# Kernel tuning notes

Hardware: AMD Instinct MI355X
Metric: run time of the kernel (lower is better)

## Reference

```python
import jax, jax.numpy as jnp
import numpy as np

EMBED_DIM = 1024
NUM_HEADS = 16
HEAD_DIM = EMBED_DIM // NUM_HEADS
SCALE = HEAD_DIM ** -0.5
B, S = 2, 2048


def setup_inputs() -> dict:
    key = jax.random.key(0)
    ks = jax.random.split(key, 10)
    def lin(kw, kb, fan_in):
        bound = 1.0 / np.sqrt(fan_in)
        W = jax.random.uniform(kw, (EMBED_DIM, EMBED_DIM), jnp.float32, -bound, bound)
        b = jax.random.uniform(kb, (EMBED_DIM,), jnp.float32, -bound, bound)
        return W, b
    Wq, bq = lin(ks[0], ks[1], EMBED_DIM)
    Wk, bk = lin(ks[2], ks[3], EMBED_DIM)
    Wv, bv = lin(ks[4], ks[5], EMBED_DIM)
    Wo, bo = lin(ks[6], ks[7], EMBED_DIM)
    x = jax.random.normal(ks[8], (B, S, EMBED_DIM), jnp.float32)
    # sparsity_mask: True where token kept (rand > sparsity with sparsity=0.5)
    sparsity_mask = jax.random.randint(ks[9], (B, NUM_HEADS, S), 0, 2).astype(bool)
    return {"x": x, "sparsity_mask": sparsity_mask,
            "Wq": Wq, "bq": bq, "Wk": Wk, "bk": bk,
            "Wv": Wv, "bv": bv, "Wo": Wo, "bo": bo}


def reference(x, sparsity_mask, Wq, bq, Wk, bk, Wv, bv, Wo, bo):
    b, s, _ = x.shape
    def heads(W, bias):
        # torch Linear: x @ W.T + b ; then [b, s, h, d] -> [b, h, s, d]
        y = x @ W.T + bias
        return y.reshape(b, s, NUM_HEADS, HEAD_DIM).transpose(0, 2, 1, 3)
    q = heads(Wq, bq)
    k = heads(Wk, bk)
    v = heads(Wv, bv)
    m = sparsity_mask[..., None].astype(q.dtype)  # [b, h, s, 1]
    q = q * m
    k = k * m
    attn = jnp.einsum('bhqd,bhkd->bhqk', q, k) * SCALE
    attn = jax.nn.softmax(attn, axis=-1)
    out = jnp.einsum('bhqk,bhkd->bhqd', attn, v)
    out = out.transpose(0, 2, 1, 3).reshape(b, s, EMBED_DIM)
    return out @ Wo.T + bo
```

## Files before the change

### kernel.cpp

```cpp
#include <hip/hip_runtime.h>

#define DEV __device__ __forceinline__

typedef __bf16 bf16x8 __attribute__((ext_vector_type(8)));
typedef __bf16 bf16x4 __attribute__((ext_vector_type(4)));
typedef float f32x4 __attribute__((ext_vector_type(4)));
typedef unsigned u32x4 __attribute__((ext_vector_type(4)));
typedef unsigned short ushort_t;

static constexpr int EMBED = 1024;
static constexpr int NHEAD = 16;
static constexpr int HDIM  = 64;
static constexpr int S_    = 2048;
static constexpr float SCALE_L2E = 0.125f * 1.44269504088896340736f;

DEV ushort_t f2bf(float f) {
  unsigned u = __builtin_bit_cast(unsigned, f);
  unsigned r = (u + 0x7fffu + ((u >> 16) & 1u)) >> 16;
  return (ushort_t)r;
}

#define GLOAD_LDS16(g, l)                                                   \
  __builtin_amdgcn_global_load_lds(                                         \
      (const __attribute__((address_space(1))) unsigned int*)(g),           \
      (__attribute__((address_space(3))) unsigned int*)(l), 16, 0, 0)

#define DRAIN_VM() asm volatile("s_waitcnt vmcnt(0)" ::: "memory")

__global__ __launch_bounds__(256) void convert_kernel(
    const float* __restrict__ x,
    const float* __restrict__ wq, const float* __restrict__ wk,
    const float* __restrict__ wv, const float* __restrict__ wo,
    ushort_t* __restrict__ xb, ushort_t* __restrict__ wqb,
    ushort_t* __restrict__ wkb, ushort_t* __restrict__ wvb,
    ushort_t* __restrict__ wob) {
  size_t i = ((size_t)blockIdx.x * blockDim.x + threadIdx.x) * 4;
  const float* src; ushort_t* dst; size_t off;
  if (i < 4194304u)      { src = x;  dst = xb;  off = i; }
  else if (i < 5242880u) { src = wq; dst = wqb; off = i - 4194304u; }
  else if (i < 6291456u) { src = wk; dst = wkb; off = i - 5242880u; }
  else if (i < 7340032u) { src = wv; dst = wvb; off = i - 6291456u; }
  else                   { src = wo; dst = wob; off = i - 7340032u; }
  float4 v = *(const float4*)(src + off);
  ushort4 o;
  o.x = f2bf(v.x); o.y = f2bf(v.y); o.z = f2bf(v.z); o.w = f2bf(v.w);
  *(ushort4*)(dst + off) = o;
}

__global__ __launch_bounds__(256) void qkv_kernel(
    const ushort_t* __restrict__ xb, const ushort_t* __restrict__ wqb,
    const ushort_t* __restrict__ wkb, const ushort_t* __restrict__ wvb,
    const float* __restrict__ bq, const float* __restrict__ bk,
    const float* __restrict__ bv, const int* __restrict__ mask,
    ushort_t* __restrict__ qo, ushort_t* __restrict__ ko,
    ushort_t* __restrict__ vto) {
  __shared__ __align__(16) unsigned char ldsA[16384];
  __shared__ __align__(16) unsigned char ldsB[16384];
  __shared__ float maskf[2][128];

  const int bid  = blockIdx.x;
  const int tid  = threadIdx.x;
  const int lane = tid & 63;
  const int w    = tid >> 6;
  const int wm   = (w >> 1) * 64;
  const int wn   = (w & 1) * 64;
  const int rl   = lane & 15;
  const int kg   = lane >> 4;

  int mode, ar0, br0;
  const ushort_t *A, *Bm;
  const float* bias;
  if (bid < 512) {
    mode = bid >> 8;
    int t = bid & 255;
    ar0 = (t & 31) * 128;
    br0 = (t >> 5) * 128;
    A = xb; Bm = mode ? wkb : wqb; bias = mode ? bk : bq;
  } else {
    mode = 2;
    int t = bid - 512;
    ar0 = (t & 7) * 128;
    br0 = (t >> 3) * 128;
    A = wvb; Bm = xb; bias = bv;
  }

  if (mode < 2) {
    int hl = tid >> 7, sl = tid & 127;
    int m = ar0 + sl;
    int b = m >> 11, s = m & 2047;
    int h = (br0 >> 6) + hl;
    maskf[hl][sl] = (float)mask[((size_t)b * NHEAD + h) * S_ + s];
  }

  f32x4 acc[4][4];
#pragma unroll
  for (int i = 0; i < 4; ++i)
#pragma unroll
    for (int j = 0; j < 4; ++j) acc[i][j] = f32x4{0.f, 0.f, 0.f, 0.f};

  auto STAGE = [&](int kt) {
    const int k0 = kt * 64;
#pragma unroll
    for (int s = 0; s < 8; ++s) {
      const int basev = s * 256 + w * 64;
      const int Lb = basev & 1023;
      const int L = Lb + lane;
      const int row = L >> 3;
      const int gu = (L & 7) ^ (row & 7);
      if (s < 4) {
        GLOAD_LDS16(A + (size_t)(ar0 + row) * EMBED + k0 + gu * 8, &ldsA[Lb * 16]);
      } else {
        GLOAD_LDS16(Bm + (size_t)(br0 + row) * EMBED + k0 + gu * 8, &ldsB[Lb * 16]);
      }
    }
  };

  for (int kt = 0; kt < 16; ++kt) {
    if (kt) __syncthreads();
    STAGE(kt);
    DRAIN_VM();
    __syncthreads();
#pragma unroll
    for (int kk = 0; kk < 2; ++kk) {
      bf16x8 af[4], bfr[4];
#pragma unroll
      for (int mb = 0; mb < 4; ++mb) {
        const int row = wm + mb * 16 + rl;
        const int off = (kk * 64 + kg * 16) ^ ((row & 7) << 4);
        af[mb] = *(const bf16x8*)(ldsA + row * 128 + off);
      }
#pragma unroll
      for (int nb = 0; nb < 4; ++nb) {
        const int row = wn + nb * 16 + rl;
        const int off = (kk * 64 + kg * 16) ^ ((row & 7) << 4);
        bfr[nb] = *(const bf16x8*)(ldsB + row * 128 + off);
      }
#pragma unroll
      for (int mb = 0; mb < 4; ++mb)
#pragma unroll
        for (int nb = 0; nb < 4; ++nb)
          acc[mb][nb] = __builtin_amdgcn_mfma_f32_16x16x32_bf16(
              af[mb], bfr[nb], acc[mb][nb], 0, 0, 0);
    }
  }

#pragma unroll
  for (int mb = 0; mb < 4; ++mb)
#pragma unroll
    for (int nb = 0; nb < 4; ++nb)
#pragma unroll
      for (int r = 0; r < 4; ++r) {
        int row_l = wm + mb * 16 + kg * 4 + r;
        int col_l = wn + nb * 16 + rl;
        float v = acc[mb][nb][r];
        if (mode < 2) {
          int m = ar0 + row_l, n = br0 + col_l;
          v = (v + bias[n]) * maskf[col_l >> 6][row_l];
          if (mode == 0) v *= SCALE_L2E;
          int b = m >> 11, s = m & 2047, h = n >> 6, d = n & 63;
          ushort_t* o = mode ? ko : qo;
          o[(((size_t)(b * NHEAD + h)) * S_ + s) * HDIM + d] = f2bf(v);
        } else {
          int n = ar0 + row_l, m = br0 + col_l;
          v += bias[n];
          int b = m >> 11, s = m & 2047, h = n >> 6, d = n & 63;
          vto[(((size_t)(b * NHEAD + h)) * HDIM + d) * S_ + s] = f2bf(v);
        }
      }
}

__global__ __launch_bounds__(256) void gemm_o_kernel(
    const ushort_t* __restrict__ A, const ushort_t* __restrict__ Bm,
    const float* __restrict__ bias, float* __restrict__ outp) {
  __shared__ __align__(16) unsigned char ldsA[16384];
  __shared__ __align__(16) unsigned char ldsB[16384];

  const int tid  = threadIdx.x;
  const int lane = tid & 63;
  const int w    = tid >> 6;
  const int ar0  = blockIdx.x * 128;
  const int br0  = blockIdx.y * 128;
  const int wm   = (w >> 1) * 64;
  const int wn   = (w & 1) * 64;
  const int rl   = lane & 15;
  const int kg   = lane >> 4;

  f32x4 acc[4][4];
#pragma unroll
  for (int i = 0; i < 4; ++i)
#pragma unroll
    for (int j = 0; j < 4; ++j) acc[i][j] = f32x4{0.f, 0.f, 0.f, 0.f};

  auto STAGE = [&](int kt) {
    const int k0 = kt * 64;
#pragma unroll
    for (int s = 0; s < 8; ++s) {
      const int basev = s * 256 + w * 64;
      const int Lb = basev & 1023;
      const int L = Lb + lane;
      const int row = L >> 3;
      const int gu = (L & 7) ^ (row & 7);
      if (s < 4) {
        GLOAD_LDS16(A + (size_t)(ar0 + row) * EMBED + k0 + gu * 8, &ldsA[Lb * 16]);
      } else {
        GLOAD_LDS16(Bm + (size_t)(br0 + row) * EMBED + k0 + gu * 8, &ldsB[Lb * 16]);
      }
    }
  };

  for (int kt = 0; kt < 16; ++kt) {
    if (kt) __syncthreads();
    STAGE(kt);
    DRAIN_VM();
    __syncthreads();
#pragma unroll
    for (int kk = 0; kk < 2; ++kk) {
      bf16x8 af[4], bfr[4];
#pragma unroll
      for (int mb = 0; mb < 4; ++mb) {
        const int row = wm + mb * 16 + rl;
        const int off = (kk * 64 + kg * 16) ^ ((row & 7) << 4);
        af[mb] = *(const bf16x8*)(ldsA + row * 128 + off);
      }
#pragma unroll
      for (int nb = 0; nb < 4; ++nb) {
        const int row = wn + nb * 16 + rl;
        const int off = (kk * 64 + kg * 16) ^ ((row & 7) << 4);
        bfr[nb] = *(const bf16x8*)(ldsB + row * 128 + off);
      }
#pragma unroll
      for (int mb = 0; mb < 4; ++mb)
#pragma unroll
        for (int nb = 0; nb < 4; ++nb)
          acc[mb][nb] = __builtin_amdgcn_mfma_f32_16x16x32_bf16(
              af[mb], bfr[nb], acc[mb][nb], 0, 0, 0);
    }
  }

#pragma unroll
  for (int mb = 0; mb < 4; ++mb)
#pragma unroll
    for (int nb = 0; nb < 4; ++nb)
#pragma unroll
      for (int r = 0; r < 4; ++r) {
        int m = ar0 + wm + mb * 16 + kg * 4 + r;
        int n = br0 + wn + nb * 16 + rl;
        outp[(size_t)m * EMBED + n] = acc[mb][nb][r] + bias[n];
      }
}

__global__ __launch_bounds__(512) void attn_kernel(
    const ushort_t* __restrict__ qp, const ushort_t* __restrict__ kp,
    const ushort_t* __restrict__ vtp, ushort_t* __restrict__ ao) {
  __shared__ __align__(16) unsigned char ldsK[3][8192];
  __shared__ __align__(16) unsigned char ldsV[3][8192];
  __shared__ __align__(16) unsigned char ldsP[8][2048];

  const int bid  = blockIdx.x;
  const int bh   = (bid & 7) * 4 + (bid >> 7);
  const int qt   = (bid >> 3) & 15;
  const int tid  = threadIdx.x;
  const int lane = tid & 63;
  const int w    = tid >> 6;
  const int q0   = qt * 128 + w * 16;
  const int rl   = lane & 15;
  const int kg   = lane >> 4;
  const int pswz = (rl & 7) << 4;

  const bf16x8 ones = __builtin_bit_cast(bf16x8,
      u32x4{0x3F803F80u, 0x3F803F80u, 0x3F803F80u, 0x3F803F80u});

  bf16x8 qa[2];
#pragma unroll
  for (int kk = 0; kk < 2; ++kk)
    qa[kk] = *(const bf16x8*)(qp + ((size_t)bh * S_ + q0 + rl) * HDIM +
                              kk * 32 + kg * 8);

  f32x4 o_acc[4];
  f32x4 o_l = f32x4{0.f, 0.f, 0.f, 0.f};
#pragma unroll
  for (int nb = 0; nb < 4; ++nb) o_acc[nb] = f32x4{0.f, 0.f, 0.f, 0.f};

  unsigned char* pb = ldsP[w];

  auto STAGE = [&](int kt, int slot) {
#pragma unroll
    for (int s = 0; s < 2; ++s) {
      const int Lb = w * 64;
      const int L = Lb + lane;
      const int row = L >> 3;
      const int gu = (L & 7) ^ (row & 7);
      if (s == 0) {
        GLOAD_LDS16(kp + ((size_t)bh * S_ + (size_t)kt * 64 + row) * HDIM + gu * 8,
                    &ldsK[slot][L * 16]);
      } else {
        GLOAD_LDS16(vtp + ((size_t)bh * HDIM + row) * S_ + (size_t)kt * 64 + gu * 8,
                    &ldsV[slot][L * 16]);
      }
    }
  };

  STAGE(0, 0);
  STAGE(1, 1);
  asm volatile("s_waitcnt vmcnt(2) lgkmcnt(0)" ::: "memory");
  __builtin_amdgcn_s_barrier();
  int cur = 0;
  for (int kt = 0; kt < 32; ++kt) {
    if (kt + 2 < 32) {
      int slot = cur + 2; if (slot >= 3) slot -= 3;
      STAGE(kt + 2, slot);
    }

    f32x4 sa[4];
#pragma unroll
    for (int nb = 0; nb < 4; ++nb) sa[nb] = f32x4{0.f, 0.f, 0.f, 0.f};
    __builtin_amdgcn_s_setprio(1);
#pragma unroll
    for (int nb = 0; nb < 4; ++nb) {
      const int row = nb * 16 + rl;
#pragma unroll
      for (int kk = 0; kk < 2; ++kk) {
        bf16x8 kf = *(const bf16x8*)(ldsK[cur] + row * 128 +
                                     ((kk * 64 + kg * 16) ^ ((row & 7) << 4)));
        sa[nb] = __builtin_amdgcn_mfma_f32_16x16x32_bf16(kf, qa[kk], sa[nb], 0, 0, 0);
      }
    }
    __builtin_amdgcn_s_setprio(0);

#pragma unroll
    for (int nb = 0; nb < 4; ++nb) {
      bf16x4 pk4;
#pragma unroll
      for (int r = 0; r < 4; ++r)
        pk4[r] = (__bf16)__builtin_amdgcn_exp2f(sa[nb][r]);
      *(bf16x4*)(pb + rl * 128 + ((nb * 32 + kg * 8) ^ pswz)) = pk4;
    }
    asm volatile("s_waitcnt lgkmcnt(0)" ::: "memory");
    __builtin_amdgcn_sched_barrier(0);

    bf16x8 pa[2];
#pragma unroll
    for (int kk = 0; kk < 2; ++kk)
      pa[kk] = *(const bf16x8*)(pb + rl * 128 + ((kk * 64 + kg * 16) ^ pswz));

    __builtin_amdgcn_s_setprio(1);
    o_l = __builtin_amdgcn_mfma_f32_16x16x32_bf16(pa[0], ones, o_l, 0, 0, 0);
    o_l = __builtin_amdgcn_mfma_f32_16x16x32_bf16(pa[1], ones, o_l, 0, 0, 0);

#pragma unroll
    for (int nb = 0; nb < 4; ++nb) {
      const int row = nb * 16 + rl;
#pragma unroll
      for (int kk = 0; kk < 2; ++kk) {
        bf16x8 vb = *(const bf16x8*)(ldsV[cur] + row * 128 +
                                     ((kk * 64 + kg * 16) ^ ((row & 7) << 4)));
        o_acc[nb] = __builtin_amdgcn_mfma_f32_16x16x32_bf16(pa[kk], vb, o_acc[nb], 0, 0, 0);
      }
    }
    __builtin_amdgcn_s_setprio(0);

    if (kt + 2 < 32) {
      asm volatile("s_waitcnt vmcnt(2) lgkmcnt(0)" ::: "memory");
    } else {
      asm volatile("s_waitcnt vmcnt(0) lgkmcnt(0)" ::: "memory");
    }
    __builtin_amdgcn_s_barrier();
    cur = (cur == 2) ? 0 : cur + 1;
  }

  const int b = bh >> 4, h = bh & 15;
#pragma unroll
  for (int r = 0; r < 4; ++r) {
    float linv = 1.0f / o_l[r];
    const int row = q0 + kg * 4 + r;
#pragma unroll
    for (int nb = 0; nb < 4; ++nb) {
      float v = o_acc[nb][r] * linv;
      ao[((size_t)b * S_ + row) * EMBED + h * HDIM + nb * 16 + rl] = f2bf(v);
    }
  }
}

extern "C" void kernel_launch(void* const* d_in, const int* in_sizes, int n_in,
                              void* d_out, int out_size, void* d_ws, size_t ws_size,
                              hipStream_t stream) {
  const float* x    = (const float*)d_in[0];
  const int*   mask = (const int*)d_in[1];
  const float* Wq   = (const float*)d_in[2];
  const float* bq   = (const float*)d_in[3];
  const float* Wk   = (const float*)d_in[4];
  const float* bk   = (const float*)d_in[5];
  const float* Wv   = (const float*)d_in[6];
  const float* bv   = (const float*)d_in[7];
  const float* Wo   = (const float*)d_in[8];
  const float* bo   = (const float*)d_in[9];

  char* ws = (char*)d_ws;
  ushort_t* xb  = (ushort_t*)(ws);
  ushort_t* wqb = (ushort_t*)(ws + 8388608);
  ushort_t* wkb = (ushort_t*)(ws + 10485760);
  ushort_t* wvb = (ushort_t*)(ws + 12582912);
  ushort_t* wob = (ushort_t*)(ws + 14680064);
  ushort_t* qb  = (ushort_t*)(ws + 16777216);
  ushort_t* kb  = (ushort_t*)(ws + 25165824);
  ushort_t* vtb = (ushort_t*)(ws + 33554432);
  ushort_t* aob = (ushort_t*)(ws + 41943040);

  hipLaunchKernelGGL(convert_kernel, dim3(8192), dim3(256), 0, stream,
                     x, Wq, Wk, Wv, Wo, xb, wqb, wkb, wvb, wob);
  hipLaunchKernelGGL(qkv_kernel, dim3(768), dim3(256), 0, stream,
                     xb, wqb, wkb, wvb, bq, bk, bv, mask, qb, kb, vtb);
  hipLaunchKernelGGL(attn_kernel, dim3(512), dim3(512), 0, stream,
                     qb, kb, vtb, aob);
  hipLaunchKernelGGL(gemm_o_kernel, dim3(32, 8), dim3(256), 0, stream,
                     aob, wob, bo, (float*)d_out);
}
```

Measured before the change: 115.2 us.

## Process two KV tiles per iteration with four-slot LDS ring buffer

The attention main loop now handles two 64-key tiles per iteration. Both QK^T products are issued up front, then the exp/write of the first tile's P is interleaved with the second tile's softmax and the PV products. The K/V LDS ring grows from three to four slots, and loads for the next pair are issued after a barrier at the end of each pair. The aim is to halve the per-tile barrier and wait overhead and give the MFMA unit more independent work to overlap with exp and LDS traffic. In exchange it raises register pressure and LDS use, and it moves the prefetch issue to the end of the compute phase.

```diff
diff --git a/kernel.cpp b/kernel.cpp
--- a/kernel.cpp
+++ b/kernel.cpp
@@ -252,8 +252,8 @@
 __global__ __launch_bounds__(512) void attn_kernel(
     const ushort_t* __restrict__ qp, const ushort_t* __restrict__ kp,
     const ushort_t* __restrict__ vtp, ushort_t* __restrict__ ao) {
-  __shared__ __align__(16) unsigned char ldsK[3][8192];
-  __shared__ __align__(16) unsigned char ldsV[3][8192];
+  __shared__ __align__(16) unsigned char ldsK[4][8192];
+  __shared__ __align__(16) unsigned char ldsV[4][8192];
   __shared__ __align__(16) unsigned char ldsP[8][2048];
 
   const int bid  = blockIdx.x;
@@ -300,33 +300,19 @@
     }
   };
 
-  STAGE(0, 0);
-  STAGE(1, 1);
-  asm volatile("s_waitcnt vmcnt(2) lgkmcnt(0)" ::: "memory");
-  __builtin_amdgcn_s_barrier();
-  int cur = 0;
-  for (int kt = 0; kt < 32; ++kt) {
-    if (kt + 2 < 32) {
-      int slot = cur + 2; if (slot >= 3) slot -= 3;
-      STAGE(kt + 2, slot);
-    }
-
-    f32x4 sa[4];
-#pragma unroll
-    for (int nb = 0; nb < 4; ++nb) sa[nb] = f32x4{0.f, 0.f, 0.f, 0.f};
-    __builtin_amdgcn_s_setprio(1);
+  auto QK = [&](int slot, f32x4 sa[4]) {
 #pragma unroll
     for (int nb = 0; nb < 4; ++nb) {
       const int row = nb * 16 + rl;
 #pragma unroll
       for (int kk = 0; kk < 2; ++kk) {
-        bf16x8 kf = *(const bf16x8*)(ldsK[cur] + row * 128 +
+        bf16x8 kf = *(const bf16x8*)(ldsK[slot] + row * 128 +
                                      ((kk * 64 + kg * 16) ^ ((row & 7) << 4)));
         sa[nb] = __builtin_amdgcn_mfma_f32_16x16x32_bf16(kf, qa[kk], sa[nb], 0, 0, 0);
       }
     }
-    __builtin_amdgcn_s_setprio(0);
-
+  };
+  auto SMW = [&](const f32x4 sa[4]) {
 #pragma unroll
     for (int nb = 0; nb < 4; ++nb) {
       bf16x4 pk4;
@@ -335,37 +321,65 @@
         pk4[r] = (__bf16)__builtin_amdgcn_exp2f(sa[nb][r]);
       *(bf16x4*)(pb + rl * 128 + ((nb * 32 + kg * 8) ^ pswz)) = pk4;
     }
+  };
+  auto PVL = [&](int slot) {
+    bf16x8 pa[2];
+#pragma unroll
+    for (int kk = 0; kk < 2; ++kk)
+      pa[kk] = *(const bf16x8*)(pb + rl * 128 + ((kk * 64 + kg * 16) ^ pswz));
+    o_l = __builtin_amdgcn_mfma_f32_16x16x32_bf16(pa[0], ones, o_l, 0, 0, 0);
+    o_l = __builtin_amdgcn_mfma_f32_16x16x32_bf16(pa[1], ones, o_l, 0, 0, 0);
+#pragma unroll
+    for (int nb = 0; nb < 4; ++nb) {
+      const int row = nb * 16 + rl;
+#pragma unroll
+      for (int kk = 0; kk < 2; ++kk) {
+        bf16x8 vb = *(const bf16x8*)(ldsV[slot] + row * 128 +
+                                     ((kk * 64 + kg * 16) ^ ((row & 7) << 4)));
+        o_acc[nb] = __builtin_amdgcn_mfma_f32_16x16x32_bf16(pa[kk], vb, o_acc[nb], 0, 0, 0);
+      }
+    }
+  };
+
+  STAGE(0, 0); STAGE(1, 1); STAGE(2, 2); STAGE(3, 3);
+  asm volatile("s_waitcnt vmcnt(4) lgkmcnt(0)" ::: "memory");
+  __builtin_amdgcn_s_barrier();
+
+  for (int kt = 0; kt < 32; kt += 2) {
+    const int s0 = kt & 3, s1 = (kt + 1) & 3;
+
+    f32x4 saA[4], saB[4];
+#pragma unroll
+    for (int nb = 0; nb < 4; ++nb) { saA[nb] = f32x4{0.f,0.f,0.f,0.f}; saB[nb] = f32x4{0.f,0.f,0.f,0.f}; }
+
+    __builtin_amdgcn_s_setprio(1);
+    QK(s0, saA);
+    QK(s1, saB);
+    __builtin_amdgcn_s_setprio(0);
+
+    SMW(saA);
     asm volatile("s_waitcnt lgkmcnt(0)" ::: "memory");
     __builtin_amdgcn_sched_barrier(0);
 
-    bf16x8 pa[2];
-#pragma unroll
-    for (int kk = 0; kk < 2; ++kk)
-      pa[kk] = *(const bf16x8*)(pb + rl * 128 + ((kk * 64 + kg * 16) ^ pswz));
-
     __builtin_amdgcn_s_setprio(1);
-    o_l = __builtin_amdgcn_mfma_f32_16x16x32_bf16(pa[0], ones, o_l, 0, 0, 0);
-    o_l = __builtin_amdgcn_mfma_f32_16x16x32_bf16(pa[1], ones, o_l, 0, 0, 0);
-
-#pragma unroll
-    for (int nb = 0; nb < 4; ++nb) {
-      const int row = nb * 16 + rl;
-#pragma unroll
-      for (int kk = 0; kk < 2; ++kk) {
-        bf16x8 vb = *(const bf16x8*)(ldsV[cur] + row * 128 +
-                                     ((kk * 64 + kg * 16) ^ ((row & 7) << 4)));
-        o_acc[nb] = __builtin_amdgcn_mfma_f32_16x16x32_bf16(pa[kk], vb, o_acc[nb], 0, 0, 0);
-      }
-    }
+    PVL(s0);
     __builtin_amdgcn_s_setprio(0);
-
-    if (kt + 2 < 32) {
-      asm volatile("s_waitcnt vmcnt(2) lgkmcnt(0)" ::: "memory");
+    SMW(saB);
+    asm volatile("s_waitcnt lgkmcnt(0)" ::: "memory");
+    __builtin_amdgcn_sched_barrier(0);
+
+    __builtin_amdgcn_s_setprio(1);
+    PVL(s1);
+    __builtin_amdgcn_s_setprio(0);
+
+    __builtin_amdgcn_s_barrier();
+    if (kt + 4 < 32) {
+      STAGE(kt + 4, s0); STAGE(kt + 5, s1);
+      asm volatile("s_waitcnt vmcnt(4) lgkmcnt(0)" ::: "memory");
     } else {
       asm volatile("s_waitcnt vmcnt(0) lgkmcnt(0)" ::: "memory");
     }
     __builtin_amdgcn_s_barrier();
-    cur = (cur == 2) ? 0 : cur + 1;
   }
 
   const int b = bh >> 4, h = bh & 15;
```

Result: faster. 111.4 us (median of 3 runs) (-3.3%).
